# Kernel tuning notes

Hardware: AMD Instinct MI355X
Metric: run time of the kernel (lower is better)

Reference implementation:

```python
import jax, jax.numpy as jnp
import numpy as np

B, NQ, NK = 4, 384, 384
D_EQUI, D_QINV, D_KVINV = 64, 256, 256
D_MSG, D_FF, D_OUT = 64, 256, 64
IN_FEATS = 2 * D_MSG + D_EQUI + D_EQUI  # q_msg + k_msg + dotprods + dists


def setup_inputs() -> dict:
    key = jax.random.key(0)
    ks = jax.random.split(key, 12)
    inp = {
        "q_equi": jax.random.normal(ks[0], (B, NQ, 3, D_EQUI), jnp.float32),
        "q_inv": jax.random.normal(ks[1], (B, NQ, D_QINV), jnp.float32),
        "k_equi": jax.random.normal(ks[2], (B, NK, 3, D_EQUI), jnp.float32),
        "k_inv": jax.random.normal(ks[3], (B, NK, D_KVINV), jnp.float32),
        # q_message_proj / k_message_proj
        "Wq": jax.random.normal(ks[4], (D_QINV, D_MSG), jnp.float32) * 0.05,
        "bq": jax.random.normal(ks[5], (D_MSG,), jnp.float32) * 0.05,
        "Wk": jax.random.normal(ks[6], (D_KVINV, D_MSG), jnp.float32) * 0.05,
        "bk": jax.random.normal(ks[7], (D_MSG,), jnp.float32) * 0.05,
        # message_mlp: Linear(in_feats, d_ff) -> SiLU -> Linear(d_ff, d_out)
        "W1": jax.random.normal(ks[8], (IN_FEATS, D_FF), jnp.float32) * 0.05,
        "b1": jax.random.normal(ks[9], (D_FF,), jnp.float32) * 0.05,
        "W2": jax.random.normal(ks[10], (D_FF, D_OUT), jnp.float32) * 0.05,
        "b2": jax.random.normal(ks[11], (D_OUT,), jnp.float32) * 0.05,
    }
    return inp


def reference(q_equi, q_inv, k_equi, k_inv, Wq, bq, Wk, bk, W1, b1, W2, b2):
    Bq, Nq = q_inv.shape[:2]
    Nk = k_inv.shape[1]
    # per-channel dot products over the 3-dim coordinate axis: [B,Nq,Nk,d_equi]
    dotprods = jnp.einsum("bqce,bkce->bqke", q_equi, k_equi)
    # message projections broadcast across the pair grid
    q_msg = q_inv @ Wq + bq  # [B,Nq,d_msg]
    k_msg = k_inv @ Wk + bk  # [B,Nk,d_msg]
    q_msg_e = jnp.broadcast_to(q_msg[:, :, None, :], (Bq, Nq, Nk, q_msg.shape[-1]))
    k_msg_e = jnp.broadcast_to(k_msg[:, None, :, :], (Bq, Nq, Nk, k_msg.shape[-1]))
    # include_dists=True: per-channel Euclidean distance over the coord axis
    vec_dists = q_equi[:, :, None, :, :] - k_equi[:, None, :, :, :]  # [B,Nq,Nk,3,d_equi]
    dists = jnp.sqrt(jnp.sum(vec_dists * vec_dists, axis=3))  # [B,Nq,Nk,d_equi]
    pairwise_feats = jnp.concatenate([q_msg_e, k_msg_e, dotprods, dists], axis=-1)
    h = jax.nn.silu(pairwise_feats @ W1 + b1)
    return h @ W2 + b2
```

## Files before the change

kernel.cpp:

```cpp
#include <hip/hip_runtime.h>

typedef __bf16 bf16;
typedef float f32x4 __attribute__((ext_vector_type(4)));
typedef bf16 bf16x8 __attribute__((ext_vector_type(8)));
typedef bf16 bf16x4 __attribute__((ext_vector_type(4)));

#define NB 4
#define NQ 384
#define NK 384
#define DE 64
#define DQI 256
#define DFF 256
#define DMSG 64
#define DOUT 64
#define KEXT 160

#define WS_AQ 0
#define WS_AK 1572864
#define WS_W1T 3145728
#define WS_W2T 3211264

__global__ __launch_bounds__(256) void prep_kernel(
    const float* __restrict__ q_inv, const float* __restrict__ k_inv,
    const float* __restrict__ Wq, const float* __restrict__ bq,
    const float* __restrict__ Wk, const float* __restrict__ bk,
    const float* __restrict__ W1, const float* __restrict__ b1,
    const float* __restrict__ W2,
    float* __restrict__ Aq, float* __restrict__ Ak,
    bf16* __restrict__ w1t, bf16* __restrict__ w2t)
{
  const int t = threadIdx.x;
  const int bid = blockIdx.x;
  if (bid < 2 * NB * NQ) {
    __shared__ float sin_[DQI];
    __shared__ float smsg[DMSG];
    const bool isQ = bid < NB * NQ;
    const int row = isQ ? bid : bid - NB * NQ;
    const float* inv = isQ ? q_inv : k_inv;
    const float* Wm = isQ ? Wq : Wk;
    const float* bm = isQ ? bq : bk;
    sin_[t] = inv[row * DQI + t];
    __syncthreads();
    if (t < DMSG) {
      float acc = bm[t];
#pragma unroll 8
      for (int d = 0; d < DQI; ++d) acc += sin_[d] * Wm[d * DMSG + t];
      smsg[t] = acc;
    }
    __syncthreads();
    {
      float acc = isQ ? b1[t] : 0.f;
      const float* w1rows = W1 + (isQ ? 0 : DMSG * DFF);
#pragma unroll 8
      for (int e = 0; e < DMSG; ++e) acc += smsg[e] * w1rows[e * DFF + t];
      (isQ ? Aq : Ak)[row * DFF + t] = acc;
    }
  } else if (bid == 2 * NB * NQ) {
    const int cs = t;
    const int c = ((cs >> 5) << 5) + (((cs >> 4) & 1) << 2) + (((cs >> 2) & 3) << 3) + (cs & 3);
    for (int k8 = 0; k8 < 16; ++k8) {
      bf16x8 v;
#pragma unroll
      for (int j = 0; j < 8; ++j) {
        int k = k8 * 8 + j;
        v[j] = (bf16)W1[(128 + k) * DFF + c];
      }
      *(bf16x8*)&w1t[cs * 128 + k8 * 8] = v;
    }
  } else {
    const int ocol = t >> 2;
    const int ksc = t & 3;
    for (int k8 = 0; k8 < 8; ++k8) {
      bf16x8 v;
#pragma unroll
      for (int j = 0; j < 8; ++j) {
        int ks = ksc * 64 + k8 * 8 + j;
        int ct = ((ks >> 5) << 5) + (((ks >> 3) & 3) << 3) + (((ks >> 2) & 1) << 2) + (ks & 3);
        v[j] = (bf16)W2[ct * DOUT + ocol];
      }
      *(bf16x8*)&w2t[ocol * 256 + ksc * 64 + k8 * 8] = v;
    }
  }
}

__global__ __launch_bounds__(256) void pair_kernel(
    const float* __restrict__ q_equi, const float* __restrict__ k_equi,
    const float* __restrict__ Aq, const float* __restrict__ Ak,
    const bf16* __restrict__ w1t, const bf16* __restrict__ w2t,
    const float* __restrict__ b2, float* __restrict__ out)
{
  __shared__ __align__(16) bf16 sA1[256 * KEXT];
  __shared__ __align__(16) bf16 sF[256 * KEXT];

  const int t = threadIdx.x;
  const int bid = blockIdx.x;
  const int b = bid / (24 * 8);
  const int rem = bid % (24 * 8);
  const int qt = rem / 8, ks = rem % 8;
  const int q0 = qt * 16;
  const int k0b = ks * 48;

  const int lane = t & 63;
  const int w = t >> 6;
  const int r16 = lane & 15;
  const int g = lane >> 4;

  {
    const bf16* src = w1t + t * 128;
    bf16* dst = sA1 + t * KEXT;
#pragma unroll
    for (int k8 = 0; k8 < 16; ++k8)
      *(bf16x8*)&dst[k8 * 8] = *(const bf16x8*)&src[k8 * 8];
  }
  {
    const int c = t;
    const int cs = ((c >> 5) << 5) + ((c & 4) << 2) + ((c & 24) >> 1) + (c & 3);
#pragma unroll
    for (int j4 = 0; j4 < 4; ++j4) {
      bf16x4 v;
#pragma unroll
      for (int j = 0; j < 4; ++j)
        v[j] = (bf16)Aq[(b * NQ + q0 + j4 * 4 + j) * DFF + c];
      *(bf16x4*)&sA1[cs * KEXT + 128 + j4 * 4] = v;
    }
  }
  {
    const int p = t;
    const int qi = p & 15, kil = p >> 4;
#pragma unroll
    for (int blk = 0; blk < 4; ++blk) {
      bf16x8 v;
#pragma unroll
      for (int e = 0; e < 8; ++e) {
        int j = blk * 8 + e;
        float x = (j < 16) ? ((j == qi) ? 1.f : 0.f) : (((j - 16) == kil) ? 1.f : 0.f);
        v[e] = (bf16)x;
      }
      *(bf16x8*)&sF[p * KEXT + 128 + blk * 8] = v;
    }
  }
  f32x4 b2v[4];
#pragma unroll
  for (int ot = 0; ot < 4; ++ot)
    b2v[ot] = *(const f32x4*)&b2[ot * 16 + g * 4];

  const int e4 = t & 15;
  const int g4 = (t >> 4) & 3;
  const int kiq = t >> 6;

  for (int it = 0; it < 3; ++it) {
    const int k0i = k0b + it * 16;
    {
      f32x4 qe[4][3], qn[4];
#pragma unroll
      for (int qii = 0; qii < 4; ++qii) {
        const int qg = b * NQ + q0 + g4 * 4 + qii;
#pragma unroll
        for (int c = 0; c < 3; ++c)
          qe[qii][c] = *(const f32x4*)&q_equi[(qg * 3 + c) * DE + e4 * 4];
        qn[qii] = qe[qii][0] * qe[qii][0] + qe[qii][1] * qe[qii][1] + qe[qii][2] * qe[qii][2];
      }
#pragma unroll
      for (int kii = 0; kii < 4; ++kii) {
        const int kil = kiq * 4 + kii;
        const int kg = b * NK + k0i + kil;
        f32x4 ke[3];
#pragma unroll
        for (int c = 0; c < 3; ++c)
          ke[c] = *(const f32x4*)&k_equi[(kg * 3 + c) * DE + e4 * 4];
        f32x4 kn = ke[0] * ke[0] + ke[1] * ke[1] + ke[2] * ke[2];
#pragma unroll
        for (int qii = 0; qii < 4; ++qii) {
          f32x4 dot = qe[qii][0] * ke[0] + qe[qii][1] * ke[1] + qe[qii][2] * ke[2];
          f32x4 d2 = qn[qii] + kn - 2.f * dot;
          const int p = kil * 16 + g4 * 4 + qii;
          bf16x4 vd, vs;
#pragma unroll
          for (int j = 0; j < 4; ++j) {
            vd[j] = (bf16)dot[j];
            float dd = d2[j] > 0.f ? d2[j] : 0.f;
            vs[j] = (bf16)__builtin_amdgcn_sqrtf(dd);
          }
          *(bf16x4*)&sF[p * KEXT + e4 * 4] = vd;
          *(bf16x4*)&sF[p * KEXT + 64 + e4 * 4] = vs;
        }
      }
      const int c = t;
      const int cs = ((c >> 5) << 5) + ((c & 4) << 2) + ((c & 24) >> 1) + (c & 3);
#pragma unroll
      for (int j4 = 0; j4 < 4; ++j4) {
        bf16x4 v;
#pragma unroll
        for (int j = 0; j < 4; ++j)
          v[j] = (bf16)Ak[(b * NK + k0i + j4 * 4 + j) * DFF + c];
        *(bf16x4*)&sA1[cs * KEXT + 144 + j4 * 4] = v;
      }
    }
    __syncthreads();
    {
      bf16x8 b1f[4][5];
#pragma unroll
      for (int pt = 0; pt < 4; ++pt)
#pragma unroll
        for (int kk = 0; kk < 5; ++kk)
          b1f[pt][kk] = *(const bf16x8*)&sF[((w * 4 + pt) * 16 + r16) * KEXT + kk * 32 + g * 8];

      f32x4 D2[4][4];
#pragma unroll
      for (int ot = 0; ot < 4; ++ot)
#pragma unroll
        for (int pt = 0; pt < 4; ++pt)
          D2[ot][pt] = (f32x4){0.f, 0.f, 0.f, 0.f};

#pragma unroll
      for (int kk2 = 0; kk2 < 8; ++kk2) {
        f32x4 dE[4], dO[4];
#pragma unroll
        for (int pt = 0; pt < 4; ++pt) {
          dE[pt] = (f32x4){0.f, 0.f, 0.f, 0.f};
          dO[pt] = (f32x4){0.f, 0.f, 0.f, 0.f};
        }
        const int ctE = kk2 * 2, ctO = kk2 * 2 + 1;
#pragma unroll
        for (int kk = 0; kk < 5; ++kk) {
          bf16x8 aE = *(const bf16x8*)&sA1[(ctE * 16 + r16) * KEXT + kk * 32 + g * 8];
#pragma unroll
          for (int pt = 0; pt < 4; ++pt)
            dE[pt] = __builtin_amdgcn_mfma_f32_16x16x32_bf16(aE, b1f[pt][kk], dE[pt], 0, 0, 0);
          bf16x8 aO = *(const bf16x8*)&sA1[(ctO * 16 + r16) * KEXT + kk * 32 + g * 8];
#pragma unroll
          for (int pt = 0; pt < 4; ++pt)
            dO[pt] = __builtin_amdgcn_mfma_f32_16x16x32_bf16(aO, b1f[pt][kk], dO[pt], 0, 0, 0);
        }
        bf16x8 a2[4];
#pragma unroll
        for (int ot = 0; ot < 4; ++ot)
          a2[ot] = *(const bf16x8*)&w2t[(ot * 16 + r16) * 256 + kk2 * 32 + g * 8];
#pragma unroll
        for (int pt = 0; pt < 4; ++pt) {
          bf16x8 b2f;
#pragma unroll
          for (int r = 0; r < 4; ++r) {
            float zE = dE[pt][r];
            float sE = zE * __builtin_amdgcn_rcpf(1.f + __builtin_amdgcn_exp2f(zE * -1.44269504f));
            b2f[r] = (bf16)sE;
            float zO = dO[pt][r];
            float sO = zO * __builtin_amdgcn_rcpf(1.f + __builtin_amdgcn_exp2f(zO * -1.44269504f));
            b2f[4 + r] = (bf16)sO;
          }
#pragma unroll
          for (int ot = 0; ot < 4; ++ot)
            D2[ot][pt] = __builtin_amdgcn_mfma_f32_16x16x32_bf16(a2[ot], b2f, D2[ot][pt], 0, 0, 0);
        }
      }
#pragma unroll
      for (int pt = 0; pt < 4; ++pt) {
        const int kg = k0i + w * 4 + pt;
        float* op = out + ((b * NQ + q0 + r16) * NK + kg) * 64 + g * 4;
#pragma unroll
        for (int ot = 0; ot < 4; ++ot) {
          f32x4 v = D2[ot][pt] + b2v[ot];
          *(f32x4*)&op[ot * 16] = v;
        }
      }
    }
    __syncthreads();
  }
}

extern "C" void kernel_launch(void* const* d_in, const int* in_sizes, int n_in,
                              void* d_out, int out_size, void* d_ws, size_t ws_size,
                              hipStream_t stream) {
  const float* q_equi = (const float*)d_in[0];
  const float* q_inv = (const float*)d_in[1];
  const float* k_equi = (const float*)d_in[2];
  const float* k_inv = (const float*)d_in[3];
  const float* Wq = (const float*)d_in[4];
  const float* bq = (const float*)d_in[5];
  const float* Wk = (const float*)d_in[6];
  const float* bk = (const float*)d_in[7];
  const float* W1 = (const float*)d_in[8];
  const float* b1 = (const float*)d_in[9];
  const float* W2 = (const float*)d_in[10];
  const float* b2 = (const float*)d_in[11];
  char* ws = (char*)d_ws;
  float* Aq = (float*)(ws + WS_AQ);
  float* Ak = (float*)(ws + WS_AK);
  bf16* w1t = (bf16*)(ws + WS_W1T);
  bf16* w2t = (bf16*)(ws + WS_W2T);
  float* out = (float*)d_out;

  prep_kernel<<<2 * NB * NQ + 2, 256, 0, stream>>>(q_inv, k_inv, Wq, bq, Wk, bk, W1, b1, W2,
                                                   Aq, Ak, w1t, w2t);
  pair_kernel<<<NB * 24 * 8, 256, 0, stream>>>(q_equi, k_equi, Aq, Ak, w1t, w2t, b2, out);
}
```

Measured before the change: 341.8 us.

## Compute pair features in registers, shrink LDS, swizzle W1 tile, transpose Aq/Ak

The pair kernel now builds the dot-product and distance B-fragments directly in registers instead of staging them through a large shared feature tile. The Aq/Ak rank-one bias terms move into a small separate LDS buffer consumed by extra MFMAs against register-resident selector fragments. The W1 tile is stored with an XOR swizzle, LDS use drops enough to allow two blocks per CU, and the prep kernel is retiled to 16 rows per block and writes transposed Aq/Ak so loads coalesce. Distances are now computed directly from differences rather than the norm expansion. The trade-off is higher register pressure under the two-block launch bound and redundant equi loads across waves.

Result: slower. 352.5 us (+3.1%).

```diff
diff --git a/kernel.cpp b/kernel.cpp
--- a/kernel.cpp
+++ b/kernel.cpp
@@ -13,10 +13,9 @@
 #define DFF 256
 #define DMSG 64
 #define DOUT 64
-#define KEXT 160
-
-#define WS_AQ 0
-#define WS_AK 1572864
+
+#define WS_AQT 0
+#define WS_AKT 1572864
 #define WS_W1T 3145728
 #define WS_W2T 3211264
 
@@ -26,36 +25,55 @@
     const float* __restrict__ Wk, const float* __restrict__ bk,
     const float* __restrict__ W1, const float* __restrict__ b1,
     const float* __restrict__ W2,
-    float* __restrict__ Aq, float* __restrict__ Ak,
+    float* __restrict__ AqT, float* __restrict__ AkT,
     bf16* __restrict__ w1t, bf16* __restrict__ w2t)
 {
   const int t = threadIdx.x;
   const int bid = blockIdx.x;
-  if (bid < 2 * NB * NQ) {
-    __shared__ float sin_[DQI];
-    __shared__ float smsg[DMSG];
-    const bool isQ = bid < NB * NQ;
-    const int row = isQ ? bid : bid - NB * NQ;
+  if (bid < 2 * NB * 24) {
+    const bool isQ = bid < NB * 24;
+    const int sub = isQ ? bid : bid - NB * 24;
+    const int b = sub / 24, tile = sub % 24;
+    const int n0 = tile * 16;
+    __shared__ float sInv[16 * 256];
+    __shared__ float sMsg[16 * 64];
     const float* inv = isQ ? q_inv : k_inv;
     const float* Wm = isQ ? Wq : Wk;
     const float* bm = isQ ? bq : bk;
-    sin_[t] = inv[row * DQI + t];
+#pragma unroll
+    for (int r = 0; r < 16; ++r)
+      sInv[r * 256 + t] = inv[(b * 384 + n0 + r) * 256 + t];
     __syncthreads();
-    if (t < DMSG) {
-      float acc = bm[t];
-#pragma unroll 8
-      for (int d = 0; d < DQI; ++d) acc += sin_[d] * Wm[d * DMSG + t];
-      smsg[t] = acc;
+    {
+      const int e = t & 63, rq = t >> 6;
+      float acc[4];
+#pragma unroll
+      for (int rr = 0; rr < 4; ++rr) acc[rr] = bm[e];
+      for (int d = 0; d < 256; ++d) {
+        float wv = Wm[d * DMSG + e];
+#pragma unroll
+        for (int rr = 0; rr < 4; ++rr) acc[rr] += sInv[(rq * 4 + rr) * 256 + d] * wv;
+      }
+#pragma unroll
+      for (int rr = 0; rr < 4; ++rr) sMsg[(rq * 4 + rr) * 64 + e] = acc[rr];
     }
     __syncthreads();
     {
-      float acc = isQ ? b1[t] : 0.f;
-      const float* w1rows = W1 + (isQ ? 0 : DMSG * DFF);
-#pragma unroll 8
-      for (int e = 0; e < DMSG; ++e) acc += smsg[e] * w1rows[e * DFF + t];
-      (isQ ? Aq : Ak)[row * DFF + t] = acc;
-    }
-  } else if (bid == 2 * NB * NQ) {
+      const int c = t;
+      const float* w1r = W1 + (isQ ? 0 : DMSG * DFF);
+      float acc[16];
+#pragma unroll
+      for (int n = 0; n < 16; ++n) acc[n] = isQ ? b1[c] : 0.f;
+      for (int e = 0; e < 64; ++e) {
+        float wv = w1r[e * DFF + c];
+#pragma unroll
+        for (int n = 0; n < 16; ++n) acc[n] += sMsg[n * 64 + e] * wv;
+      }
+      float* dst = (isQ ? AqT : AkT) + (b * 256 + c) * 384 + n0;
+#pragma unroll
+      for (int n = 0; n < 16; ++n) dst[n] = acc[n];
+    }
+  } else if (bid == 2 * NB * 24) {
     const int cs = t;
     const int c = ((cs >> 5) << 5) + (((cs >> 4) & 1) << 2) + (((cs >> 2) & 3) << 3) + (cs & 3);
     for (int k8 = 0; k8 < 16; ++k8) {
@@ -83,14 +101,14 @@
   }
 }
 
-__global__ __launch_bounds__(256) void pair_kernel(
+__global__ __launch_bounds__(256, 2) void pair_kernel(
     const float* __restrict__ q_equi, const float* __restrict__ k_equi,
-    const float* __restrict__ Aq, const float* __restrict__ Ak,
+    const float* __restrict__ AqT, const float* __restrict__ AkT,
     const bf16* __restrict__ w1t, const bf16* __restrict__ w2t,
     const float* __restrict__ b2, float* __restrict__ out)
 {
-  __shared__ __align__(16) bf16 sA1[256 * KEXT];
-  __shared__ __align__(16) bf16 sF[256 * KEXT];
+  __shared__ __align__(16) bf16 sA1[256 * 128];
+  __shared__ __align__(16) bf16 sAb[16 * 4 * 16 * 8];
 
   const int t = threadIdx.x;
   const int bid = blockIdx.x;
@@ -107,104 +125,99 @@
 
   {
     const bf16* src = w1t + t * 128;
-    bf16* dst = sA1 + t * KEXT;
+    bf16* dstrow = sA1 + t * 128;
 #pragma unroll
     for (int k8 = 0; k8 < 16; ++k8)
-      *(bf16x8*)&dst[k8 * 8] = *(const bf16x8*)&src[k8 * 8];
+      *(bf16x8*)&dstrow[((k8 ^ (t & 15)) << 3)] = *(const bf16x8*)&src[k8 * 8];
   }
   {
-    const int c = t;
-    const int cs = ((c >> 5) << 5) + ((c & 4) << 2) + ((c & 24) >> 1) + (c & 3);
-#pragma unroll
-    for (int j4 = 0; j4 < 4; ++j4) {
-      bf16x4 v;
-#pragma unroll
-      for (int j = 0; j < 4; ++j)
-        v[j] = (bf16)Aq[(b * NQ + q0 + j4 * 4 + j) * DFF + c];
-      *(bf16x4*)&sA1[cs * KEXT + 128 + j4 * 4] = v;
-    }
-  }
-  {
-    const int p = t;
-    const int qi = p & 15, kil = p >> 4;
-#pragma unroll
-    for (int blk = 0; blk < 4; ++blk) {
-      bf16x8 v;
-#pragma unroll
-      for (int e = 0; e < 8; ++e) {
-        int j = blk * 8 + e;
-        float x = (j < 16) ? ((j == qi) ? 1.f : 0.f) : (((j - 16) == kil) ? 1.f : 0.f);
-        v[e] = (bf16)x;
-      }
-      *(bf16x8*)&sF[p * KEXT + 128 + blk * 8] = v;
-    }
-  }
-  f32x4 b2v[4];
-#pragma unroll
-  for (int ot = 0; ot < 4; ++ot)
-    b2v[ot] = *(const f32x4*)&b2[ot * 16 + g * 4];
-
-  const int e4 = t & 15;
-  const int g4 = (t >> 4) & 3;
-  const int kiq = t >> 6;
+    const int c = ((t >> 5) << 5) + (((t >> 4) & 1) << 2) + (((t >> 2) & 3) << 3) + (t & 3);
+    const float* aqp = AqT + (b * 256 + c) * 384 + q0;
+    const int ct = t >> 4, rr = t & 15;
+#pragma unroll
+    for (int gg = 0; gg < 2; ++gg) {
+      f32x4 v0 = *(const f32x4*)&aqp[gg * 8];
+      f32x4 v1 = *(const f32x4*)&aqp[gg * 8 + 4];
+      bf16x8 vv;
+#pragma unroll
+      for (int j = 0; j < 4; ++j) { vv[j] = (bf16)v0[j]; vv[4 + j] = (bf16)v1[j]; }
+      *(bf16x8*)&sAb[((ct * 4 + gg) * 16 + rr) * 8] = vv;
+    }
+  }
+  bf16x8 b1sel[4];
+#pragma unroll
+  for (int pt = 0; pt < 4; ++pt) {
+#pragma unroll
+    for (int j = 0; j < 8; ++j) {
+      const int jj = g * 8 + j;
+      float v;
+      if (g < 2) v = (jj == r16) ? 1.f : 0.f;
+      else v = ((jj - 16) == (w * 4 + pt)) ? 1.f : 0.f;
+      b1sel[pt][j] = (bf16)v;
+    }
+  }
 
   for (int it = 0; it < 3; ++it) {
     const int k0i = k0b + it * 16;
-    {
-      f32x4 qe[4][3], qn[4];
-#pragma unroll
-      for (int qii = 0; qii < 4; ++qii) {
-        const int qg = b * NQ + q0 + g4 * 4 + qii;
-#pragma unroll
-        for (int c = 0; c < 3; ++c)
-          qe[qii][c] = *(const f32x4*)&q_equi[(qg * 3 + c) * DE + e4 * 4];
-        qn[qii] = qe[qii][0] * qe[qii][0] + qe[qii][1] * qe[qii][1] + qe[qii][2] * qe[qii][2];
-      }
-#pragma unroll
-      for (int kii = 0; kii < 4; ++kii) {
-        const int kil = kiq * 4 + kii;
-        const int kg = b * NK + k0i + kil;
-        f32x4 ke[3];
-#pragma unroll
-        for (int c = 0; c < 3; ++c)
-          ke[c] = *(const f32x4*)&k_equi[(kg * 3 + c) * DE + e4 * 4];
-        f32x4 kn = ke[0] * ke[0] + ke[1] * ke[1] + ke[2] * ke[2];
-#pragma unroll
-        for (int qii = 0; qii < 4; ++qii) {
-          f32x4 dot = qe[qii][0] * ke[0] + qe[qii][1] * ke[1] + qe[qii][2] * ke[2];
-          f32x4 d2 = qn[qii] + kn - 2.f * dot;
-          const int p = kil * 16 + g4 * 4 + qii;
-          bf16x4 vd, vs;
-#pragma unroll
-          for (int j = 0; j < 4; ++j) {
-            vd[j] = (bf16)dot[j];
-            float dd = d2[j] > 0.f ? d2[j] : 0.f;
-            vs[j] = (bf16)__builtin_amdgcn_sqrtf(dd);
-          }
-          *(bf16x4*)&sF[p * KEXT + e4 * 4] = vd;
-          *(bf16x4*)&sF[p * KEXT + 64 + e4 * 4] = vs;
-        }
-      }
-      const int c = t;
-      const int cs = ((c >> 5) << 5) + ((c & 4) << 2) + ((c & 24) >> 1) + (c & 3);
-#pragma unroll
-      for (int j4 = 0; j4 < 4; ++j4) {
-        bf16x4 v;
-#pragma unroll
-        for (int j = 0; j < 4; ++j)
-          v[j] = (bf16)Ak[(b * NK + k0i + j4 * 4 + j) * DFF + c];
-        *(bf16x4*)&sA1[cs * KEXT + 144 + j4 * 4] = v;
+    bf16x8 b1f[4][4];
+    {
+      const int qrow = b * NQ + q0 + r16;
+      f32x4 qv[3][4];
+#pragma unroll
+      for (int c = 0; c < 3; ++c) {
+        const float* qp = q_equi + (qrow * 3 + c) * DE;
+        qv[c][0] = *(const f32x4*)&qp[g * 8];
+        qv[c][1] = *(const f32x4*)&qp[g * 8 + 4];
+        qv[c][2] = *(const f32x4*)&qp[32 + g * 8];
+        qv[c][3] = *(const f32x4*)&qp[32 + g * 8 + 4];
+      }
+#pragma unroll
+      for (int pt = 0; pt < 4; ++pt) {
+        const int krow = b * NK + k0i + w * 4 + pt;
+        f32x4 dt[4], s2[4];
+#pragma unroll
+        for (int h = 0; h < 4; ++h) { dt[h] = (f32x4){0,0,0,0}; s2[h] = (f32x4){0,0,0,0}; }
+#pragma unroll
+        for (int c = 0; c < 3; ++c) {
+          const float* kp = k_equi + (krow * 3 + c) * DE;
+          f32x4 kv0 = *(const f32x4*)&kp[g * 8];
+          f32x4 kv1 = *(const f32x4*)&kp[g * 8 + 4];
+          f32x4 kv2 = *(const f32x4*)&kp[32 + g * 8];
+          f32x4 kv3 = *(const f32x4*)&kp[32 + g * 8 + 4];
+          dt[0] += qv[c][0] * kv0; dt[1] += qv[c][1] * kv1;
+          dt[2] += qv[c][2] * kv2; dt[3] += qv[c][3] * kv3;
+          f32x4 e0 = qv[c][0] - kv0, e1 = qv[c][1] - kv1, e2 = qv[c][2] - kv2, e3 = qv[c][3] - kv3;
+          s2[0] += e0 * e0; s2[1] += e1 * e1; s2[2] += e2 * e2; s2[3] += e3 * e3;
+        }
+        bf16x8 f0, f1, f2, f3;
+#pragma unroll
+        for (int j = 0; j < 4; ++j) {
+          f0[j] = (bf16)dt[0][j]; f0[4 + j] = (bf16)dt[1][j];
+          f1[j] = (bf16)dt[2][j]; f1[4 + j] = (bf16)dt[3][j];
+          f2[j] = (bf16)__builtin_amdgcn_sqrtf(s2[0][j]);
+          f2[4 + j] = (bf16)__builtin_amdgcn_sqrtf(s2[1][j]);
+          f3[j] = (bf16)__builtin_amdgcn_sqrtf(s2[2][j]);
+          f3[4 + j] = (bf16)__builtin_amdgcn_sqrtf(s2[3][j]);
+        }
+        b1f[pt][0] = f0; b1f[pt][1] = f1; b1f[pt][2] = f2; b1f[pt][3] = f3;
+      }
+    }
+    {
+      const int c = ((t >> 5) << 5) + (((t >> 4) & 1) << 2) + (((t >> 2) & 3) << 3) + (t & 3);
+      const float* akp = AkT + (b * 256 + c) * 384 + k0i;
+      const int ct = t >> 4, rr = t & 15;
+#pragma unroll
+      for (int gg = 2; gg < 4; ++gg) {
+        f32x4 v0 = *(const f32x4*)&akp[(gg - 2) * 8];
+        f32x4 v1 = *(const f32x4*)&akp[(gg - 2) * 8 + 4];
+        bf16x8 vv;
+#pragma unroll
+        for (int j = 0; j < 4; ++j) { vv[j] = (bf16)v0[j]; vv[4 + j] = (bf16)v1[j]; }
+        *(bf16x8*)&sAb[((ct * 4 + gg) * 16 + rr) * 8] = vv;
       }
     }
     __syncthreads();
     {
-      bf16x8 b1f[4][5];
-#pragma unroll
-      for (int pt = 0; pt < 4; ++pt)
-#pragma unroll
-        for (int kk = 0; kk < 5; ++kk)
-          b1f[pt][kk] = *(const bf16x8*)&sF[((w * 4 + pt) * 16 + r16) * KEXT + kk * 32 + g * 8];
-
       f32x4 D2[4][4];
 #pragma unroll
       for (int ot = 0; ot < 4; ++ot)
@@ -214,23 +227,32 @@
 
 #pragma unroll
       for (int kk2 = 0; kk2 < 8; ++kk2) {
+        const int ctE = kk2 * 2, ctO = kk2 * 2 + 1;
         f32x4 dE[4], dO[4];
 #pragma unroll
         for (int pt = 0; pt < 4; ++pt) {
           dE[pt] = (f32x4){0.f, 0.f, 0.f, 0.f};
           dO[pt] = (f32x4){0.f, 0.f, 0.f, 0.f};
         }
-        const int ctE = kk2 * 2, ctO = kk2 * 2 + 1;
-#pragma unroll
-        for (int kk = 0; kk < 5; ++kk) {
-          bf16x8 aE = *(const bf16x8*)&sA1[(ctE * 16 + r16) * KEXT + kk * 32 + g * 8];
+#pragma unroll
+        for (int kk = 0; kk < 4; ++kk) {
+          bf16x8 aE = *(const bf16x8*)&sA1[(ctE * 16 + r16) * 128 + (((kk * 4 + g) ^ r16) << 3)];
 #pragma unroll
           for (int pt = 0; pt < 4; ++pt)
             dE[pt] = __builtin_amdgcn_mfma_f32_16x16x32_bf16(aE, b1f[pt][kk], dE[pt], 0, 0, 0);
-          bf16x8 aO = *(const bf16x8*)&sA1[(ctO * 16 + r16) * KEXT + kk * 32 + g * 8];
+          bf16x8 aO = *(const bf16x8*)&sA1[(ctO * 16 + r16) * 128 + (((kk * 4 + g) ^ r16) << 3)];
 #pragma unroll
           for (int pt = 0; pt < 4; ++pt)
             dO[pt] = __builtin_amdgcn_mfma_f32_16x16x32_bf16(aO, b1f[pt][kk], dO[pt], 0, 0, 0);
+        }
+        {
+          bf16x8 aBE = *(const bf16x8*)&sAb[((ctE * 4 + g) * 16 + r16) * 8];
+          bf16x8 aBO = *(const bf16x8*)&sAb[((ctO * 4 + g) * 16 + r16) * 8];
+#pragma unroll
+          for (int pt = 0; pt < 4; ++pt) {
+            dE[pt] = __builtin_amdgcn_mfma_f32_16x16x32_bf16(aBE, b1sel[pt], dE[pt], 0, 0, 0);
+            dO[pt] = __builtin_amdgcn_mfma_f32_16x16x32_bf16(aBO, b1sel[pt], dO[pt], 0, 0, 0);
+          }
         }
         bf16x8 a2[4];
 #pragma unroll
@@ -253,6 +275,10 @@
             D2[ot][pt] = __builtin_amdgcn_mfma_f32_16x16x32_bf16(a2[ot], b2f, D2[ot][pt], 0, 0, 0);
         }
       }
+      f32x4 b2v[4];
+#pragma unroll
+      for (int ot = 0; ot < 4; ++ot)
+        b2v[ot] = *(const f32x4*)&b2[ot * 16 + g * 4];
 #pragma unroll
       for (int pt = 0; pt < 4; ++pt) {
         const int kg = k0i + w * 4 + pt;
@@ -284,13 +310,13 @@
   const float* W2 = (const float*)d_in[10];
   const float* b2 = (const float*)d_in[11];
   char* ws = (char*)d_ws;
-  float* Aq = (float*)(ws + WS_AQ);
-  float* Ak = (float*)(ws + WS_AK);
+  float* AqT = (float*)(ws + WS_AQT);
+  float* AkT = (float*)(ws + WS_AKT);
   bf16* w1t = (bf16*)(ws + WS_W1T);
   bf16* w2t = (bf16*)(ws + WS_W2T);
   float* out = (float*)d_out;
 
-  prep_kernel<<<2 * NB * NQ + 2, 256, 0, stream>>>(q_inv, k_inv, Wq, bq, Wk, bk, W1, b1, W2,
-                                                   Aq, Ak, w1t, w2t);
-  pair_kernel<<<NB * 24 * 8, 256, 0, stream>>>(q_equi, k_equi, Aq, Ak, w1t, w2t, b2, out);
+  prep_kernel<<<2 * NB * 24 + 2, 256, 0, stream>>>(q_inv, k_inv, Wq, bq, Wk, bk, W1, b1, W2,
+                                                   AqT, AkT, w1t, w2t);
+  pair_kernel<<<NB * 24 * 8, 256, 0, stream>>>(q_equi, k_equi, AqT, AkT, w1t, w2t, b2, out);
 }
```
